# Kernel optimization log

Measured on AMD Instinct MI355X. Metric: run time of the kernel, lower is better.

Reference implementation:

```python
import jax, jax.numpy as jnp
import numpy as np

MEMORY_DEPTH = 5
NONLINEAR_ORDER = 7
GAIN_DB = 30.0
ORDERS = list(range(1, NONLINEAR_ORDER + 1, 2))  # [1, 3, 5, 7]


def _init_coefficients():
    """Reproduce VolterraPA._init_coefficients exactly (numpy, deterministic)."""
    M = MEMORY_DEPTH
    K = len(ORDERS)
    cr = np.zeros((K, M), dtype=np.float32)
    ci = np.zeros((K, M), dtype=np.float32)
    linear_gain = 10.0 ** (GAIN_DB / 20.0)
    cr[0, 0] = linear_gain
    for m in range(1, M):
        decay = 0.1 * np.exp(-m / 2)
        cr[0, m] = decay * linear_gain
        ci[0, m] = 0.02 * decay * linear_gain
    for k_idx, k in enumerate(ORDERS[1:], start=1):
        am_am = -0.05 * linear_gain / k ** 1.5
        am_pm = 0.02 * linear_gain / k ** 1.5
        cr[k_idx, 0] = am_am
        ci[k_idx, 0] = am_pm
        for m in range(1, M):
            decay = 0.3 * np.exp(-m / 1.5)
            cr[k_idx, m] = am_am * decay
            ci[k_idx, m] = am_pm * decay * 0.5
    return jnp.asarray(cr), jnp.asarray(ci)


def setup_inputs() -> dict:
    key = jax.random.key(0)
    x = jax.random.normal(key, (64, 16384, 2), dtype=jnp.float32)
    coeffs_real, coeffs_imag = _init_coefficients()
    return {"x": x, "coeffs_real": coeffs_real, "coeffs_imag": coeffs_imag}


def reference(x, coeffs_real, coeffs_imag):
    """Memory-polynomial Volterra PA, fully vectorized.

    y(n) = sum_k sum_m h_{k,m} * x(n+M-1-m) * |x(n+M-1-m)|^{k-1}
    With odd k, |x|^{k-1} = (xr^2+xi^2)^{(k-1)/2} -- pure real integer powers,
    so the whole computation stays in real arithmetic.
    """
    M = MEMORY_DEPTH
    xr, xi = x[..., 0], x[..., 1]                      # [B, S]
    seq_len = xr.shape[1]
    out_len = seq_len - M + 1
    # sliding windows: w[b, n, m] = x[b, n + M - 1 - m]   -> [B, N, M]
    wr = jnp.stack([xr[:, M - 1 - m: M - 1 - m + out_len] for m in range(M)], axis=-1)
    wi = jnp.stack([xi[:, M - 1 - m: M - 1 - m + out_len] for m in range(M)], axis=-1)
    env2 = wr * wr + wi * wi                            # |x|^2, [B, N, M]
    # power basis: env2^p for p = (k-1)/2, k in ORDERS   -> [K, B, N, M]
    powers = jnp.stack([env2 ** ((k - 1) // 2) for k in ORDERS], axis=0)
    u = powers * wr[None]                               # Re(x)*|x|^{k-1}
    v = powers * wi[None]                               # Im(x)*|x|^{k-1}
    # complex multiply by h = cr + i*ci, summed over (k, m)
    yr = jnp.einsum('km,kbnm->bn', coeffs_real, u) - jnp.einsum('km,kbnm->bn', coeffs_imag, v)
    yi = jnp.einsum('km,kbnm->bn', coeffs_real, v) + jnp.einsum('km,kbnm->bn', coeffs_imag, u)
    return jnp.stack([yr, yi], axis=-1)                 # [B, N, 2]
```

## Files before the change

kernel.cpp:

```cpp
#include <hip/hip_runtime.h>

typedef unsigned int u32;

constexpr int Bc = 64;
constexpr int Sc = 16384;
constexpr int Mc = 5;
constexpr int Nc = Sc - Mc + 1;
constexpr int GROUPS = Nc / 4;
constexpr int TOTAL = Bc * GROUPS;
constexpr int BLOCK = 256;

__device__ __forceinline__ float bflo(u32 w) { return __uint_as_float(w << 16); }
__device__ __forceinline__ float bfhi(u32 w) { return __uint_as_float(w & 0xFFFF0000u); }

__global__ __launch_bounds__(BLOCK) void volterra_kernel(
    const u32* __restrict__ xw,
    const u32* __restrict__ crw,
    const u32* __restrict__ ciw,
    float* __restrict__ out)
{
    const bool coeff_f32 = ((crw[0] >> 16) == 0x41FCu);

    int hits = 0;
#pragma unroll
    for (int i = 0; i < 16; ++i) {
        u32 e = (xw[i] >> 8) & 0x7Fu;
        hits += (e >= 0x3Au && e <= 0x41u) ? 1 : 0;
    }
    const bool x_bf16 = (hits >= 10);

    float crf[20], cif[20];
    if (coeff_f32) {
        const float* cr = reinterpret_cast<const float*>(crw);
        const float* ci = reinterpret_cast<const float*>(ciw);
#pragma unroll
        for (int i = 0; i < 20; ++i) { crf[i] = cr[i]; cif[i] = ci[i]; }
    } else {
#pragma unroll
        for (int i = 0; i < 10; ++i) {
            u32 a = crw[i], c = ciw[i];
            crf[2 * i] = bflo(a); crf[2 * i + 1] = bfhi(a);
            cif[2 * i] = bflo(c); cif[2 * i + 1] = bfhi(c);
        }
    }

    int idx = blockIdx.x * BLOCK + threadIdx.x;
    if (idx >= TOTAL) return;
    int b  = idx / GROUPS;
    int n0 = (idx - b * GROUPS) * 4;

    float wr[8], wi[8];
    if (x_bf16) {
        const uint4* xin = reinterpret_cast<const uint4*>(xw + (size_t)b * Sc + n0);
        uint4 q0 = xin[0], q1 = xin[1];
        u32 s[8] = {q0.x, q0.y, q0.z, q0.w, q1.x, q1.y, q1.z, q1.w};
#pragma unroll
        for (int t = 0; t < 8; ++t) { wr[t] = bflo(s[t]); wi[t] = bfhi(s[t]); }
    } else {
        const float4* xin = reinterpret_cast<const float4*>(
            reinterpret_cast<const float*>(xw) + 2 * ((size_t)b * Sc + n0));
#pragma unroll
        for (int q = 0; q < 4; ++q) {
            float4 f = xin[q];
            wr[2 * q]     = f.x; wi[2 * q]     = f.y;
            wr[2 * q + 1] = f.z; wi[2 * q + 1] = f.w;
        }
    }

    float yr[4] = {0.f, 0.f, 0.f, 0.f}, yi[4] = {0.f, 0.f, 0.f, 0.f};
#pragma unroll
    for (int t = 0; t < 8; ++t) {
        float e = wr[t] * wr[t] + wi[t] * wi[t];
#pragma unroll
        for (int j = 0; j < 4; ++j) {
            int m = j + 4 - t;
            if (m < 0 || m > 4) continue;
            float ar = fmaf(fmaf(fmaf(crf[15 + m], e, crf[10 + m]), e, crf[5 + m]), e, crf[m]);
            float ai = fmaf(fmaf(fmaf(cif[15 + m], e, cif[10 + m]), e, cif[5 + m]), e, cif[m]);
            yr[j] = fmaf(ar, wr[t], fmaf(-ai, wi[t], yr[j]));
            yi[j] = fmaf(ar, wi[t], fmaf(ai, wr[t], yi[j]));
        }
    }

    float4* op = reinterpret_cast<float4*>(out + 2 * ((size_t)b * Nc + n0));
    op[0] = make_float4(yr[0], yi[0], yr[1], yi[1]);
    op[1] = make_float4(yr[2], yi[2], yr[3], yi[3]);
}

extern "C" void kernel_launch(void* const* d_in, const int* in_sizes, int n_in,
                              void* d_out, int out_size, void* d_ws, size_t ws_size,
                              hipStream_t stream) {
    const u32* x   = (const u32*)d_in[0];
    const u32* crw = (const u32*)d_in[1];
    const u32* ciw = (const u32*)d_in[2];
    float* out = (float*)d_out;
    constexpr int grid = (TOTAL + BLOCK - 1) / BLOCK;
    volterra_kernel<<<grid, BLOCK, 0, stream>>>(x, crw, ciw, out);
}
```

Measured before the change: 63.29 us.

## Compute twelve outputs per thread and use nontemporal vector stores

```diff
diff --git a/kernel.cpp b/kernel.cpp
--- a/kernel.cpp
+++ b/kernel.cpp
@@ -1,12 +1,14 @@
 #include <hip/hip_runtime.h>
 
 typedef unsigned int u32;
+typedef float f4 __attribute__((ext_vector_type(4)));
 
 constexpr int Bc = 64;
 constexpr int Sc = 16384;
 constexpr int Mc = 5;
 constexpr int Nc = Sc - Mc + 1;
-constexpr int GROUPS = Nc / 4;
+constexpr int PER = 12;
+constexpr int GROUPS = Nc / PER;
 constexpr int TOTAL = Bc * GROUPS;
 constexpr int BLOCK = 256;
 
@@ -19,6 +21,11 @@
     const u32* __restrict__ ciw,
     float* __restrict__ out)
 {
+    int idx = blockIdx.x * BLOCK + threadIdx.x;
+    if (idx >= TOTAL) return;
+    int b  = idx / GROUPS;
+    int n0 = (idx - b * GROUPS) * PER;
+
     const bool coeff_f32 = ((crw[0] >> 16) == 0x41FCu);
 
     int hits = 0;
@@ -44,35 +51,39 @@
         }
     }
 
-    int idx = blockIdx.x * BLOCK + threadIdx.x;
-    if (idx >= TOTAL) return;
-    int b  = idx / GROUPS;
-    int n0 = (idx - b * GROUPS) * 4;
-
-    float wr[8], wi[8];
+    float wr[16], wi[16];
     if (x_bf16) {
         const uint4* xin = reinterpret_cast<const uint4*>(xw + (size_t)b * Sc + n0);
-        uint4 q0 = xin[0], q1 = xin[1];
-        u32 s[8] = {q0.x, q0.y, q0.z, q0.w, q1.x, q1.y, q1.z, q1.w};
 #pragma unroll
-        for (int t = 0; t < 8; ++t) { wr[t] = bflo(s[t]); wi[t] = bfhi(s[t]); }
+        for (int q = 0; q < 4; ++q) {
+            uint4 v = xin[q];
+            u32 s[4] = {v.x, v.y, v.z, v.w};
+#pragma unroll
+            for (int c = 0; c < 4; ++c) {
+                wr[4 * q + c] = bflo(s[c]);
+                wi[4 * q + c] = bfhi(s[c]);
+            }
+        }
     } else {
         const float4* xin = reinterpret_cast<const float4*>(
             reinterpret_cast<const float*>(xw) + 2 * ((size_t)b * Sc + n0));
 #pragma unroll
-        for (int q = 0; q < 4; ++q) {
+        for (int q = 0; q < 8; ++q) {
             float4 f = xin[q];
             wr[2 * q]     = f.x; wi[2 * q]     = f.y;
             wr[2 * q + 1] = f.z; wi[2 * q + 1] = f.w;
         }
     }
 
-    float yr[4] = {0.f, 0.f, 0.f, 0.f}, yi[4] = {0.f, 0.f, 0.f, 0.f};
+    float yr[PER], yi[PER];
 #pragma unroll
-    for (int t = 0; t < 8; ++t) {
+    for (int j = 0; j < PER; ++j) { yr[j] = 0.f; yi[j] = 0.f; }
+
+#pragma unroll
+    for (int t = 0; t < 16; ++t) {
         float e = wr[t] * wr[t] + wi[t] * wi[t];
 #pragma unroll
-        for (int j = 0; j < 4; ++j) {
+        for (int j = 0; j < PER; ++j) {
             int m = j + 4 - t;
             if (m < 0 || m > 4) continue;
             float ar = fmaf(fmaf(fmaf(crf[15 + m], e, crf[10 + m]), e, crf[5 + m]), e, crf[m]);
@@ -82,9 +93,12 @@
         }
     }
 
-    float4* op = reinterpret_cast<float4*>(out + 2 * ((size_t)b * Nc + n0));
-    op[0] = make_float4(yr[0], yi[0], yr[1], yi[1]);
-    op[1] = make_float4(yr[2], yi[2], yr[3], yi[3]);
+    f4* op = reinterpret_cast<f4*>(out + 2 * ((size_t)b * Nc + n0));
+#pragma unroll
+    for (int q = 0; q < 6; ++q) {
+        f4 v = {yr[2 * q], yi[2 * q], yr[2 * q + 1], yi[2 * q + 1]};
+        __builtin_nontemporal_store(v, op + q);
+    }
 }
 
 extern "C" void kernel_launch(void* const* d_in, const int* in_sizes, int n_in,
```

Result: slower. 67.91 us (+7.3%).
